# Kernel optimization log

Hardware: AMD Instinct MI355X
Metric: run time of the kernel (lower is better)

## Reference

```python
import jax, jax.numpy as jnp
import numpy as np

N_NODES = 50000
N_EDGES = 800000
D = 128
BN_EPS = 1e-5
AGG_EPS = 1e-6


def setup_inputs() -> dict:
    key = jax.random.key(0)
    ks = jax.random.split(key, 20)
    s = 1.0 / np.sqrt(D)
    def w(k):
        return jax.random.normal(k, (D, D), jnp.float32) * s
    def b(k):
        return jax.random.normal(k, (D,), jnp.float32) * 0.01
    return {
        "x": jax.random.normal(ks[0], (N_NODES, D), jnp.float32),
        "e": jax.random.normal(ks[1], (N_EDGES, D), jnp.float32),
        "edge_index": jax.random.randint(ks[2], (2, N_EDGES), 0, N_NODES, jnp.int32),
        "WA": w(ks[3]), "bA": b(ks[4]),
        "WB": w(ks[5]), "bB": b(ks[6]),
        "WC": w(ks[7]), "bC": b(ks[8]),
        "WD": w(ks[9]), "bD": b(ks[10]),
        "WE": w(ks[11]), "bE": b(ks[12]),
        "gamma_x": jnp.ones((D,), jnp.float32), "beta_x": jnp.zeros((D,), jnp.float32),
        "gamma_e": jnp.ones((D,), jnp.float32), "beta_e": jnp.zeros((D,), jnp.float32),
    }


def _batchnorm(v, gamma, beta):
    # training-mode BatchNorm1d: batch stats, biased variance
    mean = v.mean(axis=0)
    var = v.var(axis=0)
    return gamma * (v - mean) * jax.lax.rsqrt(var + BN_EPS) + beta


def reference(x, e, edge_index, WA, bA, WB, bB, WC, bC, WD, bD, WE, bE,
              gamma_x, beta_x, gamma_e, beta_e):
    n_nodes = x.shape[0]
    src = edge_index[0]  # x_j (source)
    dst = edge_index[1]  # x_i (target), aggregation index

    Ax = x @ WA + bA
    Bx = x @ WB + bB
    Ce = e @ WC + bC
    Dx = x @ WD + bD
    Ex = x @ WE + bE

    # message: gather endpoints, gate
    e_ij = Dx[dst] + Ex[src] + Ce            # [n_edges, D]
    sigma_ij = jax.nn.sigmoid(e_ij)

    # aggregate: scatter-sum numerator & denominator, normalize
    num = jax.ops.segment_sum(sigma_ij * Bx[src], dst, num_segments=n_nodes)
    den = jax.ops.segment_sum(sigma_ij, dst, num_segments=n_nodes)
    aggr = num / (den + AGG_EPS)

    # update + BN + ReLU (dropout=0, residual=False per GraphGym wrapper)
    x_out = jax.nn.relu(_batchnorm(Ax + aggr, gamma_x, beta_x))
    e_out = jax.nn.relu(_batchnorm(e_ij, gamma_e, beta_e))
    return x_out, e_out
```

## Files before the change

### kernel.cpp

```cpp
#include <hip/hip_runtime.h>
#include <stdint.h>

#define DD 128
#define NB_G 2048

using f32x4  = __attribute__((ext_vector_type(4))) float;
using bf16x8 = __attribute__((ext_vector_type(8))) short;

__device__ __forceinline__ float bf2f(short u) {
  union { unsigned int i; float f; } c;
  c.i = ((unsigned int)(unsigned short)u) << 16;
  return c.f;
}
__device__ __forceinline__ short f2bf(float f) {
  union { float f; unsigned int i; } c;
  c.f = f;
  unsigned int u = c.i;
  u += 0x7fffu + ((u >> 16) & 1u);
  return (short)(u >> 16);
}

__global__ __launch_bounds__(256) void k_hist(const int* __restrict__ dst, int* __restrict__ deg, int E) {
  int e = blockIdx.x * 256 + threadIdx.x;
  if (e < E) atomicAdd(&deg[dst[e]], 1);
}

__global__ __launch_bounds__(256) void k_scan1(const int* __restrict__ deg, int* __restrict__ off,
                                               int* __restrict__ totals, int n) {
  __shared__ int sm[256];
  int t = threadIdx.x;
  int i = blockIdx.x * 256 + t;
  int v = (i < n) ? deg[i] : 0;
  sm[t] = v;
  __syncthreads();
  int acc = v;
  #pragma unroll
  for (int d = 1; d < 256; d <<= 1) {
    int add = (t >= d) ? sm[t - d] : 0;
    __syncthreads();
    acc += add;
    sm[t] = acc;
    __syncthreads();
  }
  if (i < n) off[i] = acc - v;
  if (t == 255) totals[blockIdx.x] = acc;
}

__global__ __launch_bounds__(256) void k_scan2(const int* __restrict__ totals, int* __restrict__ boff, int nb) {
  __shared__ int sm[256];
  int t = threadIdx.x;
  int v = (t < nb) ? totals[t] : 0;
  sm[t] = v;
  __syncthreads();
  int acc = v;
  #pragma unroll
  for (int d = 1; d < 256; d <<= 1) {
    int add = (t >= d) ? sm[t - d] : 0;
    __syncthreads();
    acc += add;
    sm[t] = acc;
    __syncthreads();
  }
  boff[t] = acc - v;
}

__global__ __launch_bounds__(256) void k_scan3(int* __restrict__ off, const int* __restrict__ boff,
                                               int* __restrict__ cursor, int n) {
  int i = blockIdx.x * 256 + threadIdx.x;
  if (i < n) {
    int o = off[i] + boff[blockIdx.x];
    off[i] = o;
    cursor[i] = o;
  }
}

__global__ __launch_bounds__(256) void k_fill(const int* __restrict__ dst, const int* __restrict__ src,
                                              int* __restrict__ cursor, int* __restrict__ list,
                                              int* __restrict__ srcS, int E) {
  int e = blockIdx.x * 256 + threadIdx.x;
  if (e < E) {
    int p = atomicAdd(&cursor[dst[e]], 1);
    list[p] = e;
    srcS[p] = src[e];
  }
}

__global__ __launch_bounds__(256) void k_prewt5(
    const float* __restrict__ WA, const float* __restrict__ WB, const float* __restrict__ WC,
    const float* __restrict__ WD, const float* __restrict__ WE,
    short* __restrict__ WtA, short* __restrict__ WtB, short* __restrict__ WtC,
    short* __restrict__ WtD, short* __restrict__ WtE) {
  const float* Ws[5] = {WA, WB, WC, WD, WE};
  short* Os[5] = {WtA, WtB, WtC, WtD, WtE};
  const float* W = Ws[blockIdx.x];
  short* O = Os[blockIdx.x];
  int t = threadIdx.x, c = t & 127, h = t >> 7;
  for (int p = 0; p < 8; ++p) {
    int k0 = (h * 8 + p) * 8;
    bf16x8 v;
    #pragma unroll
    for (int j = 0; j < 8; ++j) v[j] = f2bf(W[(size_t)(k0 + j) * DD + c]);
    *(bf16x8*)&O[(size_t)c * DD + k0] = v;
  }
}

__global__ __launch_bounds__(256) void k_nodegemm(
    const float* __restrict__ x,
    const short* __restrict__ WtA, const float* __restrict__ bA,
    const short* __restrict__ WtB, const float* __restrict__ bB,
    const short* __restrict__ WtD, const float* __restrict__ bD,
    const short* __restrict__ WtE, const float* __restrict__ bE,
    short* __restrict__ Axh, short* __restrict__ Bxh,
    short* __restrict__ Dxh, short* __restrict__ Exh, int n) {
  int t = threadIdx.x;
  int w = t >> 6, l = t & 63, lg = l >> 4, lc = l & 15;
  int m0 = blockIdx.x * 64;
  int row = m0 + w * 16 + lc;
  bool valid = row < n;
  int rowc = valid ? row : n - 1;

  const float* xr = x + (size_t)rowc * DD;
  bf16x8 af[4];
  #pragma unroll
  for (int kk = 0; kk < 4; ++kk) {
    float4 a0 = *(const float4*)&xr[kk * 32 + lg * 8];
    float4 a1 = *(const float4*)&xr[kk * 32 + lg * 8 + 4];
    af[kk][0] = f2bf(a0.x); af[kk][1] = f2bf(a0.y); af[kk][2] = f2bf(a0.z); af[kk][3] = f2bf(a0.w);
    af[kk][4] = f2bf(a1.x); af[kk][5] = f2bf(a1.y); af[kk][6] = f2bf(a1.z); af[kk][7] = f2bf(a1.w);
  }

  const short* Wt[4] = {WtA, WtB, WtD, WtE};
  const float* bs[4] = {bA, bB, bD, bE};
  short* Os[4] = {Axh, Bxh, Dxh, Exh};

  #pragma unroll
  for (int mi = 0; mi < 4; ++mi) {
    const short* Wm = Wt[mi];
    f32x4 acc[8] = {};
    #pragma unroll
    for (int kk = 0; kk < 4; ++kk) {
      #pragma unroll
      for (int tt = 0; tt < 8; ++tt) {
        bf16x8 bfv = *(const bf16x8*)&Wm[(size_t)(tt * 16 + lc) * DD + kk * 32 + lg * 8];
        acc[tt] = __builtin_amdgcn_mfma_f32_16x16x32_bf16(bfv, af[kk], acc[tt], 0, 0, 0);
      }
    }
    if (valid) {
      short* O = Os[mi];
      #pragma unroll
      for (int tt = 0; tt < 8; ++tt) {
        int f0 = tt * 16 + lg * 4;
        float4 bc = *(const float4*)&bs[mi][f0];
        short4 o;
        o.x = f2bf(acc[tt][0] + bc.x);
        o.y = f2bf(acc[tt][1] + bc.y);
        o.z = f2bf(acc[tt][2] + bc.z);
        o.w = f2bf(acc[tt][3] + bc.w);
        *(short4*)&O[(size_t)row * DD + f0] = o;
      }
    }
  }
}

__global__ __launch_bounds__(256) void k_edge(
    const float* __restrict__ e, const short* __restrict__ WtC, const float* __restrict__ bC,
    const int* __restrict__ srcI, const int* __restrict__ dstI,
    const short* __restrict__ Dxh, const short* __restrict__ Exh,
    short* __restrict__ eij, float* __restrict__ pE, int Etot) {
  __shared__ __align__(16) short es[4][16][136];
  __shared__ float sE[4][128], qE[4][128];
  int t = threadIdx.x;
  int w = t >> 6, l = t & 63, lg = l >> 4, lc = l & 15;
  size_t m0 = (size_t)blockIdx.x * 64;

  bf16x8 dv[4], sv[4];
  bool vz[4];
  #pragma unroll
  for (int z = 0; z < 4; ++z) {
    size_t erow = m0 + w * 16 + z * 4 + lg;
    vz[z] = erow < (size_t)Etot;
    size_t erc = vz[z] ? erow : (size_t)(Etot - 1);
    int dn = dstI[erc], sn = srcI[erc];
    dv[z] = *(const bf16x8*)&Dxh[(size_t)dn * DD + lc * 8];
    sv[z] = *(const bf16x8*)&Exh[(size_t)sn * DD + lc * 8];
  }

  size_t row = m0 + w * 16 + lc;
  size_t rowc = row < (size_t)Etot ? row : (size_t)(Etot - 1);
  const float* er = e + rowc * DD;
  bf16x8 af[4];
  #pragma unroll
  for (int kk = 0; kk < 4; ++kk) {
    float4 a0 = *(const float4*)&er[kk * 32 + lg * 8];
    float4 a1 = *(const float4*)&er[kk * 32 + lg * 8 + 4];
    af[kk][0] = f2bf(a0.x); af[kk][1] = f2bf(a0.y); af[kk][2] = f2bf(a0.z); af[kk][3] = f2bf(a0.w);
    af[kk][4] = f2bf(a1.x); af[kk][5] = f2bf(a1.y); af[kk][6] = f2bf(a1.z); af[kk][7] = f2bf(a1.w);
  }

  f32x4 acc[8] = {};
  #pragma unroll
  for (int kk = 0; kk < 4; ++kk) {
    #pragma unroll
    for (int tt = 0; tt < 8; ++tt) {
      bf16x8 bfv = *(const bf16x8*)&WtC[(size_t)(tt * 16 + lc) * DD + kk * 32 + lg * 8];
      acc[tt] = __builtin_amdgcn_mfma_f32_16x16x32_bf16(af[kk], bfv, acc[tt], 0, 0, 0);
    }
  }

  float bCv[8];
  #pragma unroll
  for (int tt = 0; tt < 8; ++tt) bCv[tt] = bC[tt * 16 + lc];

  #pragma unroll
  for (int tt = 0; tt < 8; ++tt) {
    int col = tt * 16 + lc;
    #pragma unroll
    for (int j = 0; j < 4; ++j)
      es[w][lg * 4 + j][col] = f2bf(acc[tt][j] + bCv[tt]);
  }
  asm volatile("s_waitcnt lgkmcnt(0)" ::: "memory");
  __builtin_amdgcn_sched_barrier(0);

  float se[8] = {}, qe[8] = {};
  #pragma unroll
  for (int z = 0; z < 4; ++z) {
    if (vz[z]) {
      int r = z * 4 + lg;
      size_t erow = m0 + w * 16 + r;
      bf16x8 cv = *(const bf16x8*)&es[w][r][lc * 8];
      bf16x8 o;
      #pragma unroll
      for (int j = 0; j < 8; ++j) {
        float v = bf2f(cv[j]) + bf2f(dv[z][j]) + bf2f(sv[z][j]);
        se[j] += v; qe[j] += v * v;
        o[j] = f2bf(v);
      }
      *(bf16x8*)&eij[erow * DD + lc * 8] = o;
    }
  }
  __builtin_amdgcn_sched_barrier(0);

  #pragma unroll
  for (int j = 0; j < 8; ++j) {
    se[j] += __shfl_xor(se[j], 16); se[j] += __shfl_xor(se[j], 32);
    qe[j] += __shfl_xor(qe[j], 16); qe[j] += __shfl_xor(qe[j], 32);
  }
  if (lg == 0) {
    #pragma unroll
    for (int j = 0; j < 8; ++j) { sE[w][lc * 8 + j] = se[j]; qE[w][lc * 8 + j] = qe[j]; }
  }
  __syncthreads();
  if (t < 128) {
    float a = sE[0][t] + sE[1][t] + sE[2][t] + sE[3][t];
    float b = qE[0][t] + qE[1][t] + qE[2][t] + qE[3][t];
    pE[(size_t)blockIdx.x * 256 + t] = a;
    pE[(size_t)blockIdx.x * 256 + 128 + t] = b;
  }
}

__global__ __launch_bounds__(256) void k_gather(
    const int* __restrict__ off, const int* __restrict__ deg, const int* __restrict__ list,
    const int* __restrict__ srcS, const short* __restrict__ eij, const short* __restrict__ Bxh,
    const short* __restrict__ Axh, const float* __restrict__ stE,
    float* __restrict__ outx, float* __restrict__ oute,
    float* __restrict__ pX, int n) {
  int t = threadIdx.x;
  int w = t >> 6, l = t & 63;
  int qw = l >> 4, fi = l & 15;
  int waveId = blockIdx.x * 4 + w;
  const int nwaves = NB_G * 4;

  float su[8], hu[8];
  {
    float4 s0 = *(const float4*)&stE[fi * 8], s1 = *(const float4*)&stE[fi * 8 + 4];
    float4 h0 = *(const float4*)&stE[128 + fi * 8], h1 = *(const float4*)&stE[128 + fi * 8 + 4];
    su[0] = s0.x; su[1] = s0.y; su[2] = s0.z; su[3] = s0.w;
    su[4] = s1.x; su[5] = s1.y; su[6] = s1.z; su[7] = s1.w;
    hu[0] = h0.x; hu[1] = h0.y; hu[2] = h0.z; hu[3] = h0.w;
    hu[4] = h1.x; hu[5] = h1.y; hu[6] = h1.z; hu[7] = h1.w;
  }

  float sx[4] = {}, qx[4] = {};

  for (int node = waveId; node < n; node += nwaves) {
    int start = off[node], dg = deg[node];
    float num[8] = {}, den[8] = {};
    int k = qw;
    for (; k + 4 < dg; k += 8) {
      int p0 = start + k, p1 = start + k + 4;
      int id0 = list[p0], id1 = list[p1];
      int s0 = srcS[p0], s1 = srcS[p1];
      bf16x8 e0 = *(const bf16x8*)&eij[(size_t)id0 * DD + fi * 8];
      bf16x8 e1 = *(const bf16x8*)&eij[(size_t)id1 * DD + fi * 8];
      bf16x8 b0 = *(const bf16x8*)&Bxh[(size_t)s0 * DD + fi * 8];
      bf16x8 b1 = *(const bf16x8*)&Bxh[(size_t)s1 * DD + fi * 8];
      float4 oa, ob, oc, od;
      float v0a[8], v1a[8];
      #pragma unroll
      for (int j = 0; j < 8; ++j) {
        float v0 = bf2f(e0[j]), v1 = bf2f(e1[j]);
        v0a[j] = fmaxf(0.f, v0 * su[j] + hu[j]);
        v1a[j] = fmaxf(0.f, v1 * su[j] + hu[j]);
        float g0 = 1.f / (1.f + __expf(-v0)), g1 = 1.f / (1.f + __expf(-v1));
        num[j] += g0 * bf2f(b0[j]) + g1 * bf2f(b1[j]);
        den[j] += g0 + g1;
      }
      oa.x = v0a[0]; oa.y = v0a[1]; oa.z = v0a[2]; oa.w = v0a[3];
      ob.x = v0a[4]; ob.y = v0a[5]; ob.z = v0a[6]; ob.w = v0a[7];
      oc.x = v1a[0]; oc.y = v1a[1]; oc.z = v1a[2]; oc.w = v1a[3];
      od.x = v1a[4]; od.y = v1a[5]; od.z = v1a[6]; od.w = v1a[7];
      *(float4*)&oute[(size_t)id0 * DD + fi * 8] = oa;
      *(float4*)&oute[(size_t)id0 * DD + fi * 8 + 4] = ob;
      *(float4*)&oute[(size_t)id1 * DD + fi * 8] = oc;
      *(float4*)&oute[(size_t)id1 * DD + fi * 8 + 4] = od;
    }
    for (; k < dg; k += 4) {
      int p0 = start + k;
      int id0 = list[p0];
      int s0 = srcS[p0];
      bf16x8 e0 = *(const bf16x8*)&eij[(size_t)id0 * DD + fi * 8];
      bf16x8 b0 = *(const bf16x8*)&Bxh[(size_t)s0 * DD + fi * 8];
      float4 oa, ob;
      float v0a[8];
      #pragma unroll
      for (int j = 0; j < 8; ++j) {
        float v0 = bf2f(e0[j]);
        v0a[j] = fmaxf(0.f, v0 * su[j] + hu[j]);
        float g0 = 1.f / (1.f + __expf(-v0));
        num[j] += g0 * bf2f(b0[j]);
        den[j] += g0;
      }
      oa.x = v0a[0]; oa.y = v0a[1]; oa.z = v0a[2]; oa.w = v0a[3];
      ob.x = v0a[4]; ob.y = v0a[5]; ob.z = v0a[6]; ob.w = v0a[7];
      *(float4*)&oute[(size_t)id0 * DD + fi * 8] = oa;
      *(float4*)&oute[(size_t)id0 * DD + fi * 8 + 4] = ob;
    }
    #pragma unroll
    for (int j = 0; j < 8; ++j) {
      num[j] += __shfl_xor(num[j], 16); num[j] += __shfl_xor(num[j], 32);
      den[j] += __shfl_xor(den[j], 16); den[j] += __shfl_xor(den[j], 32);
    }
    if (qw < 2) {
      int c0 = fi * 8 + qw * 4;
      short4 ax = *(const short4*)&Axh[(size_t)node * DD + c0];
      short axa[4] = {ax.x, ax.y, ax.z, ax.w};
      float4 o;
      float vv[4];
      #pragma unroll
      for (int j = 0; j < 4; ++j) {
        int jj = qw * 4 + j;
        float aggr = num[jj] / (den[jj] + 1e-6f);
        float xp = bf2f(axa[j]) + aggr;
        vv[j] = xp;
        sx[j] += xp; qx[j] += xp * xp;
      }
      o.x = vv[0]; o.y = vv[1]; o.z = vv[2]; o.w = vv[3];
      *(float4*)&outx[(size_t)node * DD + c0] = o;
    }
  }

  __shared__ float lsX[4][128], lqX[4][128];
  if (qw < 2) {
    #pragma unroll
    for (int j = 0; j < 4; ++j) { lsX[w][fi * 8 + qw * 4 + j] = sx[j]; lqX[w][fi * 8 + qw * 4 + j] = qx[j]; }
  }
  __syncthreads();
  if (t < 128) {
    float a = lsX[0][t] + lsX[1][t] + lsX[2][t] + lsX[3][t];
    float b = lqX[0][t] + lqX[1][t] + lqX[2][t] + lqX[3][t];
    pX[(size_t)blockIdx.x * 256 + t] = a;
    pX[(size_t)blockIdx.x * 256 + 128 + t] = b;
  }
}

__global__ __launch_bounds__(256) void k_reduce(const float* __restrict__ part, int nblk, float invcnt,
                                                const float* __restrict__ gamma, const float* __restrict__ beta,
                                                float* __restrict__ stats) {
  int c = blockIdx.x, t = threadIdx.x;
  float a = 0.f, b = 0.f;
  for (int k = t; k < nblk; k += 256) {
    a += part[(size_t)k * 256 + c];
    b += part[(size_t)k * 256 + 128 + c];
  }
  #pragma unroll
  for (int o = 32; o > 0; o >>= 1) { a += __shfl_down(a, o); b += __shfl_down(b, o); }
  __shared__ float ra[4], rb[4];
  int l = t & 63, w = t >> 6;
  if (l == 0) { ra[w] = a; rb[w] = b; }
  __syncthreads();
  if (t == 0) {
    a = ra[0] + ra[1] + ra[2] + ra[3];
    b = rb[0] + rb[1] + rb[2] + rb[3];
    float mean = a * invcnt;
    float var = b * invcnt - mean * mean;
    float istd = rsqrtf(var + 1e-5f);
    float scale = gamma[c] * istd;
    stats[c] = scale;
    stats[128 + c] = beta[c] - mean * scale;
  }
}

__global__ __launch_bounds__(256) void k_xfinal(float* __restrict__ v, const float* __restrict__ st, size_t n4) {
  size_t i = (size_t)blockIdx.x * 256 + threadIdx.x;
  if (i >= n4) return;
  float4 d = *(const float4*)&v[i * 4];
  int f0 = (int)((i * 4) & 127);
  d.x = fmaxf(0.f, d.x * st[f0 + 0] + st[128 + f0 + 0]);
  d.y = fmaxf(0.f, d.y * st[f0 + 1] + st[128 + f0 + 1]);
  d.z = fmaxf(0.f, d.z * st[f0 + 2] + st[128 + f0 + 2]);
  d.w = fmaxf(0.f, d.w * st[f0 + 3] + st[128 + f0 + 3]);
  *(float4*)&v[i * 4] = d;
}

extern "C" void kernel_launch(void* const* d_in, const int* in_sizes, int n_in,
                              void* d_out, int out_size, void* d_ws, size_t ws_size,
                              hipStream_t stream) {
  const float* x  = (const float*)d_in[0];
  const float* e  = (const float*)d_in[1];
  const int*   ei = (const int*)d_in[2];
  const float* WA = (const float*)d_in[3];  const float* bA = (const float*)d_in[4];
  const float* WB = (const float*)d_in[5];  const float* bB = (const float*)d_in[6];
  const float* WC = (const float*)d_in[7];  const float* bC = (const float*)d_in[8];
  const float* WD = (const float*)d_in[9];  const float* bD = (const float*)d_in[10];
  const float* WE = (const float*)d_in[11]; const float* bE = (const float*)d_in[12];
  const float* gx = (const float*)d_in[13]; const float* bx = (const float*)d_in[14];
  const float* ge = (const float*)d_in[15]; const float* be = (const float*)d_in[16];

  int N = in_sizes[0] / DD;
  int E = in_sizes[2] / 2;
  const int* srcI = ei;
  const int* dstI = ei + E;

  float* outx = (float*)d_out;
  float* oute = (float*)d_out + (size_t)N * DD;

  int ntilesE = (E + 63) / 64;

  char* wp = (char*)d_ws;
  auto alloc = [&](size_t sz) { char* p = wp; wp += (sz + 255) & ~(size_t)255; return p; };
  short* Axh    = (short*)alloc((size_t)N * DD * 2);
  short* Bxh    = (short*)alloc((size_t)N * DD * 2);
  short* Dxh    = (short*)alloc((size_t)N * DD * 2);
  short* Exh    = (short*)alloc((size_t)N * DD * 2);
  short* eij    = (short*)alloc((size_t)E * DD * 2);
  int*   deg    = (int*)alloc((size_t)N * 4);
  int*   off    = (int*)alloc((size_t)N * 4);
  int*   cursor = (int*)alloc((size_t)N * 4);
  int*   totals = (int*)alloc(1024);
  int*   boff   = (int*)alloc(1024);
  int*   list   = (int*)alloc((size_t)E * 4);
  int*   srcS   = (int*)alloc((size_t)E * 4);
  float* pE     = (float*)alloc((size_t)ntilesE * 256 * 4);
  float* pX     = (float*)alloc((size_t)NB_G * 256 * 4);
  float* statsE = (float*)alloc(1024);
  float* statsX = (float*)alloc(1024);
  short* WtA    = (short*)alloc((size_t)DD * DD * 2);
  short* WtB    = (short*)alloc((size_t)DD * DD * 2);
  short* WtC    = (short*)alloc((size_t)DD * DD * 2);
  short* WtD    = (short*)alloc((size_t)DD * DD * 2);
  short* WtE    = (short*)alloc((size_t)DD * DD * 2);
  (void)ws_size; (void)n_in; (void)out_size;

  int nsb = (N + 255) / 256;

  hipMemsetAsync(deg, 0, (size_t)N * 4, stream);
  k_prewt5<<<5, 256, 0, stream>>>(WA, WB, WC, WD, WE, WtA, WtB, WtC, WtD, WtE);
  k_hist<<<(E + 255) / 256, 256, 0, stream>>>(dstI, deg, E);
  k_scan1<<<nsb, 256, 0, stream>>>(deg, off, totals, N);
  k_scan2<<<1, 256, 0, stream>>>(totals, boff, nsb);
  k_scan3<<<nsb, 256, 0, stream>>>(off, boff, cursor, N);
  k_fill<<<(E + 255) / 256, 256, 0, stream>>>(dstI, srcI, cursor, list, srcS, E);

  k_nodegemm<<<(N + 63) / 64, 256, 0, stream>>>(x, WtA, bA, WtB, bB, WtD, bD, WtE, bE,
                                                Axh, Bxh, Dxh, Exh, N);
  k_edge<<<ntilesE, 256, 0, stream>>>(e, WtC, bC, srcI, dstI, Dxh, Exh, eij, pE, E);
  k_reduce<<<128, 256, 0, stream>>>(pE, ntilesE, 1.0f / (float)E, ge, be, statsE);

  k_gather<<<NB_G, 256, 0, stream>>>(off, deg, list, srcS, eij, Bxh, Axh, statsE,
                                     outx, oute, pX, N);
  k_reduce<<<128, 256, 0, stream>>>(pX, NB_G, 1.0f / (float)N, gx, bx, statsX);
  k_xfinal<<<(int)(((size_t)N * DD / 4 + 255) / 256), 256, 0, stream>>>(outx, statsX, (size_t)N * DD / 4);
}
```

Measured before the change: 694.9 us.

## Store edge features in dst-sorted order and make edge kernel persistent with prefetch

```diff
diff --git a/kernel.cpp b/kernel.cpp
--- a/kernel.cpp
+++ b/kernel.cpp
@@ -3,6 +3,7 @@
 
 #define DD 128
 #define NB_G 2048
+#define GE   2048
 
 using f32x4  = __attribute__((ext_vector_type(4))) float;
 using bf16x8 = __attribute__((ext_vector_type(8))) short;
@@ -76,12 +77,13 @@
 
 __global__ __launch_bounds__(256) void k_fill(const int* __restrict__ dst, const int* __restrict__ src,
                                               int* __restrict__ cursor, int* __restrict__ list,
-                                              int* __restrict__ srcS, int E) {
+                                              int* __restrict__ srcS, int* __restrict__ posOf, int E) {
   int e = blockIdx.x * 256 + threadIdx.x;
   if (e < E) {
     int p = atomicAdd(&cursor[dst[e]], 1);
     list[p] = e;
     srcS[p] = src[e];
+    posOf[e] = p;
   }
 }
 
@@ -164,81 +166,122 @@
 
 __global__ __launch_bounds__(256) void k_edge(
     const float* __restrict__ e, const short* __restrict__ WtC, const float* __restrict__ bC,
-    const int* __restrict__ srcI, const int* __restrict__ dstI,
+    const int* __restrict__ srcI, const int* __restrict__ dstI, const int* __restrict__ posOf,
     const short* __restrict__ Dxh, const short* __restrict__ Exh,
-    short* __restrict__ eij, float* __restrict__ pE, int Etot) {
+    short* __restrict__ eijS, float* __restrict__ pE, int Etot, int ntiles) {
   __shared__ __align__(16) short es[4][16][136];
   __shared__ float sE[4][128], qE[4][128];
   int t = threadIdx.x;
   int w = t >> 6, l = t & 63, lg = l >> 4, lc = l & 15;
-  size_t m0 = (size_t)blockIdx.x * 64;
-
-  bf16x8 dv[4], sv[4];
-  bool vz[4];
-  #pragma unroll
-  for (int z = 0; z < 4; ++z) {
-    size_t erow = m0 + w * 16 + z * 4 + lg;
-    vz[z] = erow < (size_t)Etot;
-    size_t erc = vz[z] ? erow : (size_t)(Etot - 1);
-    int dn = dstI[erc], sn = srcI[erc];
-    dv[z] = *(const bf16x8*)&Dxh[(size_t)dn * DD + lc * 8];
-    sv[z] = *(const bf16x8*)&Exh[(size_t)sn * DD + lc * 8];
-  }
-
-  size_t row = m0 + w * 16 + lc;
-  size_t rowc = row < (size_t)Etot ? row : (size_t)(Etot - 1);
-  const float* er = e + rowc * DD;
-  bf16x8 af[4];
-  #pragma unroll
-  for (int kk = 0; kk < 4; ++kk) {
-    float4 a0 = *(const float4*)&er[kk * 32 + lg * 8];
-    float4 a1 = *(const float4*)&er[kk * 32 + lg * 8 + 4];
-    af[kk][0] = f2bf(a0.x); af[kk][1] = f2bf(a0.y); af[kk][2] = f2bf(a0.z); af[kk][3] = f2bf(a0.w);
-    af[kk][4] = f2bf(a1.x); af[kk][5] = f2bf(a1.y); af[kk][6] = f2bf(a1.z); af[kk][7] = f2bf(a1.w);
-  }
-
-  f32x4 acc[8] = {};
-  #pragma unroll
-  for (int kk = 0; kk < 4; ++kk) {
+
+  float bCv[8];
+  #pragma unroll
+  for (int tt = 0; tt < 8; ++tt) bCv[tt] = bC[tt * 16 + lc];
+
+  float se[8] = {}, qe[8] = {};
+
+  const int stride = gridDim.x;
+  int tile = blockIdx.x;
+
+  float4 e32[8];
+  int dnN[4], snN[4], posN[4];
+
+  {
+    size_t m0 = (size_t)tile * 64;
+    size_t row = m0 + w * 16 + lc;
+    if (row >= (size_t)Etot) row = Etot - 1;
+    const float* er = e + row * DD;
+    #pragma unroll
+    for (int kk = 0; kk < 4; ++kk) {
+      e32[kk * 2]     = *(const float4*)&er[kk * 32 + lg * 8];
+      e32[kk * 2 + 1] = *(const float4*)&er[kk * 32 + lg * 8 + 4];
+    }
+    #pragma unroll
+    for (int z = 0; z < 4; ++z) {
+      size_t erow = m0 + w * 16 + z * 4 + lg;
+      if (erow >= (size_t)Etot) erow = Etot - 1;
+      dnN[z] = dstI[erow]; snN[z] = srcI[erow]; posN[z] = posOf[erow];
+    }
+  }
+
+  for (; tile < ntiles; tile += stride) {
+    int dn[4], sn[4], pos[4];
+    #pragma unroll
+    for (int z = 0; z < 4; ++z) { dn[z] = dnN[z]; sn[z] = snN[z]; pos[z] = posN[z]; }
+
+    bf16x8 dv[4], sv[4];
+    #pragma unroll
+    for (int z = 0; z < 4; ++z) {
+      dv[z] = *(const bf16x8*)&Dxh[(size_t)dn[z] * DD + lc * 8];
+      sv[z] = *(const bf16x8*)&Exh[(size_t)sn[z] * DD + lc * 8];
+    }
+
+    bf16x8 af[4];
+    #pragma unroll
+    for (int kk = 0; kk < 4; ++kk) {
+      float4 a0 = e32[kk * 2], a1 = e32[kk * 2 + 1];
+      af[kk][0] = f2bf(a0.x); af[kk][1] = f2bf(a0.y); af[kk][2] = f2bf(a0.z); af[kk][3] = f2bf(a0.w);
+      af[kk][4] = f2bf(a1.x); af[kk][5] = f2bf(a1.y); af[kk][6] = f2bf(a1.z); af[kk][7] = f2bf(a1.w);
+    }
+
+    int nt = tile + stride;
+    if (nt < ntiles) {
+      size_t m0n = (size_t)nt * 64;
+      size_t row = m0n + w * 16 + lc;
+      if (row >= (size_t)Etot) row = Etot - 1;
+      const float* er = e + row * DD;
+      #pragma unroll
+      for (int kk = 0; kk < 4; ++kk) {
+        e32[kk * 2]     = *(const float4*)&er[kk * 32 + lg * 8];
+        e32[kk * 2 + 1] = *(const float4*)&er[kk * 32 + lg * 8 + 4];
+      }
+      #pragma unroll
+      for (int z = 0; z < 4; ++z) {
+        size_t erow = m0n + w * 16 + z * 4 + lg;
+        if (erow >= (size_t)Etot) erow = Etot - 1;
+        dnN[z] = dstI[erow]; snN[z] = srcI[erow]; posN[z] = posOf[erow];
+      }
+    }
+
+    f32x4 acc[8] = {};
+    #pragma unroll
+    for (int kk = 0; kk < 4; ++kk) {
+      #pragma unroll
+      for (int tt = 0; tt < 8; ++tt) {
+        bf16x8 bfv = *(const bf16x8*)&WtC[(size_t)(tt * 16 + lc) * DD + kk * 32 + lg * 8];
+        acc[tt] = __builtin_amdgcn_mfma_f32_16x16x32_bf16(af[kk], bfv, acc[tt], 0, 0, 0);
+      }
+    }
+
     #pragma unroll
     for (int tt = 0; tt < 8; ++tt) {
-      bf16x8 bfv = *(const bf16x8*)&WtC[(size_t)(tt * 16 + lc) * DD + kk * 32 + lg * 8];
-      acc[tt] = __builtin_amdgcn_mfma_f32_16x16x32_bf16(af[kk], bfv, acc[tt], 0, 0, 0);
-    }
-  }
-
-  float bCv[8];
-  #pragma unroll
-  for (int tt = 0; tt < 8; ++tt) bCv[tt] = bC[tt * 16 + lc];
-
-  #pragma unroll
-  for (int tt = 0; tt < 8; ++tt) {
-    int col = tt * 16 + lc;
-    #pragma unroll
-    for (int j = 0; j < 4; ++j)
-      es[w][lg * 4 + j][col] = f2bf(acc[tt][j] + bCv[tt]);
-  }
-  asm volatile("s_waitcnt lgkmcnt(0)" ::: "memory");
-  __builtin_amdgcn_sched_barrier(0);
-
-  float se[8] = {}, qe[8] = {};
-  #pragma unroll
-  for (int z = 0; z < 4; ++z) {
-    if (vz[z]) {
-      int r = z * 4 + lg;
-      size_t erow = m0 + w * 16 + r;
-      bf16x8 cv = *(const bf16x8*)&es[w][r][lc * 8];
-      bf16x8 o;
-      #pragma unroll
-      for (int j = 0; j < 8; ++j) {
-        float v = bf2f(cv[j]) + bf2f(dv[z][j]) + bf2f(sv[z][j]);
-        se[j] += v; qe[j] += v * v;
-        o[j] = f2bf(v);
-      }
-      *(bf16x8*)&eij[erow * DD + lc * 8] = o;
-    }
-  }
-  __builtin_amdgcn_sched_barrier(0);
+      int col = tt * 16 + lc;
+      #pragma unroll
+      for (int j = 0; j < 4; ++j)
+        es[w][lg * 4 + j][col] = f2bf(acc[tt][j] + bCv[tt]);
+    }
+    asm volatile("s_waitcnt lgkmcnt(0)" ::: "memory");
+    __builtin_amdgcn_sched_barrier(0);
+
+    size_t m0 = (size_t)tile * 64;
+    #pragma unroll
+    for (int z = 0; z < 4; ++z) {
+      size_t erow = m0 + w * 16 + z * 4 + lg;
+      if (erow < (size_t)Etot) {
+        int r = z * 4 + lg;
+        bf16x8 cv = *(const bf16x8*)&es[w][r][lc * 8];
+        bf16x8 o;
+        #pragma unroll
+        for (int j = 0; j < 8; ++j) {
+          float v = bf2f(cv[j]) + bf2f(dv[z][j]) + bf2f(sv[z][j]);
+          se[j] += v; qe[j] += v * v;
+          o[j] = f2bf(v);
+        }
+        *(bf16x8*)&eijS[(size_t)pos[z] * DD + lc * 8] = o;
+      }
+    }
+    __builtin_amdgcn_sched_barrier(0);
+  }
 
   #pragma unroll
   for (int j = 0; j < 8; ++j) {
@@ -260,7 +303,7 @@
 
 __global__ __launch_bounds__(256) void k_gather(
     const int* __restrict__ off, const int* __restrict__ deg, const int* __restrict__ list,
-    const int* __restrict__ srcS, const short* __restrict__ eij, const short* __restrict__ Bxh,
+    const int* __restrict__ srcS, const short* __restrict__ eijS, const short* __restrict__ Bxh,
     const short* __restrict__ Axh, const float* __restrict__ stE,
     float* __restrict__ outx, float* __restrict__ oute,
     float* __restrict__ pX, int n) {
@@ -290,8 +333,8 @@
       int p0 = start + k, p1 = start + k + 4;
       int id0 = list[p0], id1 = list[p1];
       int s0 = srcS[p0], s1 = srcS[p1];
-      bf16x8 e0 = *(const bf16x8*)&eij[(size_t)id0 * DD + fi * 8];
-      bf16x8 e1 = *(const bf16x8*)&eij[(size_t)id1 * DD + fi * 8];
+      bf16x8 e0 = *(const bf16x8*)&eijS[(size_t)p0 * DD + fi * 8];
+      bf16x8 e1 = *(const bf16x8*)&eijS[(size_t)p1 * DD + fi * 8];
       bf16x8 b0 = *(const bf16x8*)&Bxh[(size_t)s0 * DD + fi * 8];
       bf16x8 b1 = *(const bf16x8*)&Bxh[(size_t)s1 * DD + fi * 8];
       float4 oa, ob, oc, od;
@@ -318,7 +361,7 @@
       int p0 = start + k;
       int id0 = list[p0];
       int s0 = srcS[p0];
-      bf16x8 e0 = *(const bf16x8*)&eij[(size_t)id0 * DD + fi * 8];
+      bf16x8 e0 = *(const bf16x8*)&eijS[(size_t)p0 * DD + fi * 8];
       bf16x8 b0 = *(const bf16x8*)&Bxh[(size_t)s0 * DD + fi * 8];
       float4 oa, ob;
       float v0a[8];
@@ -442,7 +485,7 @@
   short* Bxh    = (short*)alloc((size_t)N * DD * 2);
   short* Dxh    = (short*)alloc((size_t)N * DD * 2);
   short* Exh    = (short*)alloc((size_t)N * DD * 2);
-  short* eij    = (short*)alloc((size_t)E * DD * 2);
+  short* eijS   = (short*)alloc((size_t)E * DD * 2);
   int*   deg    = (int*)alloc((size_t)N * 4);
   int*   off    = (int*)alloc((size_t)N * 4);
   int*   cursor = (int*)alloc((size_t)N * 4);
@@ -450,7 +493,8 @@
   int*   boff   = (int*)alloc(1024);
   int*   list   = (int*)alloc((size_t)E * 4);
   int*   srcS   = (int*)alloc((size_t)E * 4);
-  float* pE     = (float*)alloc((size_t)ntilesE * 256 * 4);
+  int*   posOf  = (int*)alloc((size_t)E * 4);
+  float* pE     = (float*)alloc((size_t)GE * 256 * 4);
   float* pX     = (float*)alloc((size_t)NB_G * 256 * 4);
   float* statsE = (float*)alloc(1024);
   float* statsX = (float*)alloc(1024);
@@ -469,14 +513,14 @@
   k_scan1<<<nsb, 256, 0, stream>>>(deg, off, totals, N);
   k_scan2<<<1, 256, 0, stream>>>(totals, boff, nsb);
   k_scan3<<<nsb, 256, 0, stream>>>(off, boff, cursor, N);
-  k_fill<<<(E + 255) / 256, 256, 0, stream>>>(dstI, srcI, cursor, list, srcS, E);
+  k_fill<<<(E + 255) / 256, 256, 0, stream>>>(dstI, srcI, cursor, list, srcS, posOf, E);
 
   k_nodegemm<<<(N + 63) / 64, 256, 0, stream>>>(x, WtA, bA, WtB, bB, WtD, bD, WtE, bE,
                                                 Axh, Bxh, Dxh, Exh, N);
-  k_edge<<<ntilesE, 256, 0, stream>>>(e, WtC, bC, srcI, dstI, Dxh, Exh, eij, pE, E);
-  k_reduce<<<128, 256, 0, stream>>>(pE, ntilesE, 1.0f / (float)E, ge, be, statsE);
-
-  k_gather<<<NB_G, 256, 0, stream>>>(off, deg, list, srcS, eij, Bxh, Axh, statsE,
+  k_edge<<<GE, 256, 0, stream>>>(e, WtC, bC, srcI, dstI, posOf, Dxh, Exh, eijS, pE, E, ntilesE);
+  k_reduce<<<128, 256, 0, stream>>>(pE, GE, 1.0f / (float)E, ge, be, statsE);
+
+  k_gather<<<NB_G, 256, 0, stream>>>(off, deg, list, srcS, eijS, Bxh, Axh, statsE,
                                      outx, oute, pX, N);
   k_reduce<<<128, 256, 0, stream>>>(pX, NB_G, 1.0f / (float)N, gx, bx, statsX);
   k_xfinal<<<(int)(((size_t)N * DD / 4 + 255) / 256), 256, 0, stream>>>(outx, statsX, (size_t)N * DD / 4);
```

After: 599.4 us. 1.16x faster.
